# Optimization experiments

Measured on AMD Instinct MI355X. Metric: run time of the kernel, lower is better.

## Reference

```python
import jax, jax.numpy as jnp
import numpy as np

D = 1024
H = 16
HD = D // H  # 64


def setup_inputs() -> dict:
    key = jax.random.key(0)
    ks = jax.random.split(key, 10)
    s = 0.02
    return {
        "x": jax.random.normal(ks[0], (2, 2048, D), dtype=jnp.float32),
        "rel_bias": jax.random.normal(ks[1], (H, 2048, 2048), dtype=jnp.float32),
        "Wq": jax.random.normal(ks[2], (D, D), dtype=jnp.float32) * s,
        "bq": jnp.zeros((D,), dtype=jnp.float32),
        "Wk": jax.random.normal(ks[3], (D, D), dtype=jnp.float32) * s,
        "bk": jnp.zeros((D,), dtype=jnp.float32),
        "Wv": jax.random.normal(ks[4], (D, D), dtype=jnp.float32) * s,
        "bv": jnp.zeros((D,), dtype=jnp.float32),
        "Wo": jax.random.normal(ks[5], (D, D), dtype=jnp.float32) * s,
        "bo": jnp.zeros((D,), dtype=jnp.float32),
    }


def reference(x, rel_bias, Wq, bq, Wk, bk, Wv, bv, Wo, bo):
    B, L, _ = x.shape
    # QKV projections -> [B, H, L, HD]
    def proj(W, b):
        return (x @ W.T + b).reshape(B, L, H, HD).transpose(0, 2, 1, 3)
    q = proj(Wq, bq)
    k = proj(Wk, bk)
    v = proj(Wv, bv)
    scale = 1.0 / jnp.sqrt(jnp.float32(HD))
    scores = jnp.einsum("bhqd,bhkd->bhqk", q, k) * scale + rel_bias[None]
    attn = jax.nn.softmax(scores, axis=-1)  # dropout p=0 -> identity
    out = jnp.einsum("bhqk,bhkd->bhqd", attn, v)
    out = out.transpose(0, 2, 1, 3).reshape(B, L, H * HD)
    return out @ Wo.T + bo
```

## Files before the change

### kernel.cpp

```cpp
#include <hip/hip_runtime.h>


typedef __attribute__((ext_vector_type(8))) short bf16x8;
typedef __attribute__((ext_vector_type(4))) float f32x4;
typedef __attribute__((ext_vector_type(16))) float f32x16;
typedef __attribute__((ext_vector_type(8))) unsigned short u16x8;
using u16 = unsigned short;

#define MFMA16(a, b, c) __builtin_amdgcn_mfma_f32_16x16x32_bf16((a), (b), (c), 0, 0, 0)
#define MFMA32(a, b, c) __builtin_amdgcn_mfma_f32_32x32x16_bf16((a), (b), (c), 0, 0, 0)
#define LOG2E 1.44269504088896f
#define QSCALE (0.125f * 1.44269504088896f)

__device__ __forceinline__ u16 f2bf(float f) {
  union { float f; unsigned int u; } v; v.f = f;
  unsigned int r = v.u + 0x7FFFu + ((v.u >> 16) & 1u);
  return (u16)(r >> 16);
}

__device__ __forceinline__ unsigned cvt_pk_bf16(float lo, float hi) {
  unsigned r;
  asm volatile("v_cvt_pk_bf16_f32 %0, %1, %2" : "=v"(r) : "v"(lo), "v"(hi));
  return r;
}

__device__ __forceinline__ void pl32swap(unsigned& a, unsigned& b) {
#if __has_builtin(__builtin_amdgcn_permlane32_swap)
  typedef unsigned pl2 __attribute__((ext_vector_type(2)));
  pl2 r = __builtin_amdgcn_permlane32_swap(a, b, false, false);
  a = r[0];
  b = r[1];
#else
  asm volatile("v_permlane32_swap_b32 %0, %1" : "+v"(a), "+v"(b));
#endif
}

__device__ __forceinline__ void g2lds16(const void* gsrc, void* ldst) {
  __builtin_amdgcn_global_load_lds(
      (const __attribute__((address_space(1))) unsigned int*)gsrc,
      (__attribute__((address_space(3))) unsigned int*)ldst, 16, 0, 0);
}

__global__ __launch_bounds__(256) void cvt_all(
    const float* __restrict__ x, const float* __restrict__ wq,
    const float* __restrict__ wk, const float* __restrict__ wv,
    const float* __restrict__ wo, u16* __restrict__ xb,
    u16* __restrict__ w1b, u16* __restrict__ wob) {
  int bid = blockIdx.x, tid = threadIdx.x;
  const float* src; u16* dst; int i;
  if (bid < 2048)      { src = x;  dst = xb;            i = bid * 256 + tid; }
  else if (bid < 2560) { src = wq; dst = w1b;           i = (bid - 2048) * 256 + tid; }
  else if (bid < 3072) { src = wk; dst = w1b + (1<<20); i = (bid - 2560) * 256 + tid; }
  else if (bid < 3584) { src = wv; dst = w1b + (2<<20); i = (bid - 3072) * 256 + tid; }
  else                 { src = wo; dst = wob;           i = (bid - 3584) * 256 + tid; }
  const float4* s = (const float4*)src;
  float4 a = s[2 * i], b = s[2 * i + 1];
  u16x8 o;
  o[0] = f2bf(a.x); o[1] = f2bf(a.y); o[2] = f2bf(a.z); o[3] = f2bf(a.w);
  o[4] = f2bf(b.x); o[5] = f2bf(b.y); o[6] = f2bf(b.z); o[7] = f2bf(b.w);
  ((u16x8*)dst)[i] = o;
}

template <int MODE>
__global__ __launch_bounds__(256, 2) void gemm_bt(
    const u16* __restrict__ A, const u16* __restrict__ B,
    u16* __restrict__ qp, u16* __restrict__ kp, u16* __restrict__ vp,
    const float* __restrict__ b0, const float* __restrict__ b1,
    const float* __restrict__ b2, float* __restrict__ outp,
    const float* __restrict__ bo) {
  __shared__ __align__(16) u16 lA[128 * 64];
  __shared__ __align__(16) u16 lB[128 * 64];
  const int tid = threadIdx.x;
  const int lane = tid & 63, wid = tid >> 6;
  const int g = lane >> 4, cc = lane & 15;
  const int wr = wid >> 1, wc = wid & 1;
  const int m0 = blockIdx.y * 128, n0 = blockIdx.x * 128;
  f32x4 acc[4][4] = {};
  for (int kt = 0; kt < 16; ++kt) {
    const int kof = kt * 64;
#pragma unroll
    for (int i = 0; i < 4; ++i) {
      int cid = i * 256 + tid;
      int row = cid >> 3;
      int col = (cid & 7) * 8;
      g2lds16(A + (size_t)(m0 + row) * 1024 + kof + col, &lA[(i * 256 + wid * 64) * 8]);
      g2lds16(B + (size_t)(n0 + row) * 1024 + kof + col, &lB[(i * 256 + wid * 64) * 8]);
    }
    __syncthreads();
#pragma unroll
    for (int kc = 0; kc < 2; ++kc) {
      bf16x8 af[4], bfr[4];
#pragma unroll
      for (int mf = 0; mf < 4; ++mf)
        af[mf] = *(const bf16x8*)&lA[(wr * 64 + mf * 16 + cc) * 64 + kc * 32 + g * 8];
#pragma unroll
      for (int nf = 0; nf < 4; ++nf)
        bfr[nf] = *(const bf16x8*)&lB[(wc * 64 + nf * 16 + cc) * 64 + kc * 32 + g * 8];
#pragma unroll
      for (int mf = 0; mf < 4; ++mf)
#pragma unroll
        for (int nf = 0; nf < 4; ++nf)
          acc[mf][nf] = MFMA16(af[mf], bfr[nf], acc[mf][nf]);
    }
    __syncthreads();
  }
#pragma unroll
  for (int mf = 0; mf < 4; ++mf) {
#pragma unroll
    for (int nf = 0; nf < 4; ++nf) {
      int n = n0 + wc * 64 + nf * 16 + cc;
      if (MODE == 0) {
        int which = n >> 10;
        int nn = n & 1023;
        const float* bp = which == 0 ? b0 : (which == 1 ? b1 : b2);
        float bias = bp[nn];
        int h = nn >> 6, hd = nn & 63;
        int mb = m0 + wr * 64 + mf * 16 + g * 4;
        int bb = mb >> 11, ll0 = mb & 2047;
        if (which == 2) {
          ushort4 pk4;
          pk4.x = f2bf(acc[mf][nf][0] + bias);
          pk4.y = f2bf(acc[mf][nf][1] + bias);
          pk4.z = f2bf(acc[mf][nf][2] + bias);
          pk4.w = f2bf(acc[mf][nf][3] + bias);
          *(ushort4*)&vp[(((size_t)(bb * 16 + h)) * 64 + hd) * 2048 + ll0] = pk4;
        } else {
          u16* dp = which == 0 ? qp : kp;
#pragma unroll
          for (int r = 0; r < 4; ++r) {
            float val = acc[mf][nf][r] + bias;
            if (which == 0) val *= QSCALE;
            dp[(((size_t)(bb * 16 + h)) * 2048 + ll0 + r) * 64 + hd] = f2bf(val);
          }
        }
      } else {
        float bias = bo[n];
#pragma unroll
        for (int r = 0; r < 4; ++r) {
          int m = m0 + wr * 64 + mf * 16 + g * 4 + r;
          outp[(size_t)m * 1024 + n] = acc[mf][nf][r] + bias;
        }
      }
    }
  }
}

__global__ __launch_bounds__(256, 2) void attn_kernel(
    const u16* __restrict__ qm, const u16* __restrict__ km,
    const u16* __restrict__ vtm, const float* __restrict__ bias,
    u16* __restrict__ aout) {
  __shared__ __align__(16) u16 lK[2][4096];
  __shared__ __align__(16) u16 lV[2][4096];
  const int tid = threadIdx.x;
  const int lane = tid & 63, wid = tid >> 6;
  const int lq = lane & 31, hi = lane >> 5;
  const int lin = blockIdx.x;
  const int xcd = lin & 7, j = lin >> 3;
  const int h = xcd * 2 + (j >> 5);
  const int rem = j & 31;
  const int b = rem >> 4, qb = rem & 15;
  const int q0w = qb * 128 + wid * 32;
  const size_t bh = (size_t)b * 16 + h;
  const u16* kg = km + bh * 2048 * 64;
  const u16* vg = vtm + bh * 64 * 2048;
  const u16* qbase = qm + (bh * 2048 + q0w) * 64;
  const float* brow = bias + ((size_t)h * 2048 + q0w + lq) * 2048 + 4 * hi;

  bf16x8 qf[4];
#pragma unroll
  for (int i = 0; i < 4; ++i)
    qf[i] = *(const bf16x8*)&qbase[(size_t)lq * 64 + i * 16 + 8 * hi];

  f32x16 o[2];
#pragma unroll
  for (int r = 0; r < 16; ++r) { o[0][r] = 0.f; o[1][r] = 0.f; }
  float lsum = 0.f;

#define STAGE_TILE(gbase, rs, ldst)                                            \
  _Pragma("unroll") for (int rep = 0; rep < 2; ++rep) {                        \
    int i = rep * 256 + tid;                                                   \
    int row = i >> 3, pcol = i & 7;                                            \
    int lcol = pcol ^ (row & 7);                                               \
    g2lds16((gbase) + (size_t)row * (rs) + lcol * 8, (ldst) + i * 8);          \
  }

#define SUBTILE(s_, BC, PP)                                                    \
  {                                                                            \
    f32x16 acc;                                                                \
    _Pragma("unroll") for (int r = 0; r < 16; ++r) acc[r] = -32.0f;            \
    _Pragma("unroll") for (int i = 0; i < 4; ++i) {                            \
      int row = (s_) * 32 + lq;                                                \
      bf16x8 kf = *(const bf16x8*)&lK[PP][row * 64 + (((2 * i + hi) ^ (row & 7))) * 8]; \
      acc = MFMA32(kf, qf[i], acc);                                            \
    }                                                                          \
    _Pragma("unroll") for (int r = 0; r < 16; ++r)                             \
      acc[r] = fmaf(BC[(s_) * 4 + (r >> 2)][r & 3], LOG2E, acc[r]);            \
    float p[16];                                                               \
    _Pragma("unroll") for (int r = 0; r < 16; ++r) {                           \
      p[r] = __builtin_amdgcn_exp2f(acc[r]);                                   \
      lsum += p[r];                                                            \
    }                                                                          \
    unsigned c0 = cvt_pk_bf16(p[0], p[1]),   c1 = cvt_pk_bf16(p[2], p[3]);     \
    unsigned c2 = cvt_pk_bf16(p[4], p[5]),   c3 = cvt_pk_bf16(p[6], p[7]);     \
    unsigned c4 = cvt_pk_bf16(p[8], p[9]),   c5 = cvt_pk_bf16(p[10], p[11]);   \
    unsigned c6 = cvt_pk_bf16(p[12], p[13]), c7 = cvt_pk_bf16(p[14], p[15]);   \
    pl32swap(c0, c2); pl32swap(c1, c3);                   \
    pl32swap(c4, c6); pl32swap(c5, c7);                  \
    union { unsigned u[4]; bf16x8 v; } a0, a1;                                 \
    a0.u[0] = c0; a0.u[1] = c1; a0.u[2] = c2; a0.u[3] = c3;                    \
    a1.u[0] = c4; a1.u[1] = c5; a1.u[2] = c6; a1.u[3] = c7;                    \
    _Pragma("unroll") for (int dblk = 0; dblk < 2; ++dblk) {                   \
      int rowv = dblk * 32 + lq;                                               \
      bf16x8 v0 = *(const bf16x8*)&lV[PP][rowv * 64 + (((4 * (s_) + hi) ^ (rowv & 7))) * 8];     \
      bf16x8 v1 = *(const bf16x8*)&lV[PP][rowv * 64 + (((4 * (s_) + 2 + hi) ^ (rowv & 7))) * 8]; \
      o[dblk] = MFMA32(a0.v, v0, o[dblk]);                                     \
      o[dblk] = MFMA32(a1.v, v1, o[dblk]);                                     \
    }                                                                          \
  }

  float4 bA[8], bB[8];
  STAGE_TILE(kg, 64, (u16*)lK[0])
  STAGE_TILE(vg, 2048, (u16*)lV[0])
  __builtin_amdgcn_sched_barrier(0);
#pragma unroll
  for (int gi = 0; gi < 8; ++gi) {
    bA[gi] = *(const float4*)(brow + (gi >> 2) * 32 + (gi & 3) * 8);
    bB[gi] = *(const float4*)(brow + 64 + (gi >> 2) * 32 + (gi & 3) * 8);
  }
  __builtin_amdgcn_sched_barrier(0);
  asm volatile("s_waitcnt vmcnt(8)" ::: "memory");
  __builtin_amdgcn_sched_barrier(0);
  __builtin_amdgcn_s_barrier();
  __builtin_amdgcn_sched_barrier(0);

#define ATTN_STEP(kt_, BC, DOSTAGE, DOBIAS)                                    \
  {                                                                            \
    const int k0 = (kt_) * 64;                                                 \
    const int PP = (kt_) & 1;                                                  \
    if (DOSTAGE) {                                                             \
      STAGE_TILE(kg + (size_t)(k0 + 64) * 64, 64, (u16*)lK[PP ^ 1])            \
      STAGE_TILE(vg + (k0 + 64), 2048, (u16*)lV[PP ^ 1])                       \
    }                                                                          \
    __builtin_amdgcn_sched_barrier(0);                                         \
    SUBTILE(0, BC, PP)                                                         \
    SUBTILE(1, BC, PP)                                                         \
                          \
    if (DOBIAS) {                                                              \
      _Pragma("unroll") for (int gi = 0; gi < 8; ++gi)                         \
          BC[gi] = *(const float4*)(brow + k0 + 128 + (gi >> 2) * 32 + (gi & 3) * 8); \
    }                                                                          \
    __builtin_amdgcn_sched_barrier(0);                                         \
    if (DOSTAGE && DOBIAS) { asm volatile("s_waitcnt vmcnt(8)" ::: "memory"); }\
    else                   { asm volatile("s_waitcnt vmcnt(0)" ::: "memory"); }\
    __builtin_amdgcn_sched_barrier(0);                                         \
    if (DOSTAGE) { __builtin_amdgcn_s_barrier(); }                             \
    __builtin_amdgcn_sched_barrier(0);                                         \
  }

#pragma unroll 1
  for (int kt = 0; kt < 30; kt += 2) {
    ATTN_STEP(kt, bA, 1, 1)
    ATTN_STEP(kt + 1, bB, 1, 1)
  }
  ATTN_STEP(30, bA, 1, 0)
  ATTN_STEP(31, bB, 0, 0)
#undef ATTN_STEP
#undef SUBTILE
#undef STAGE_TILE

  lsum += __shfl_xor(lsum, 32, 64);
  float linv = 1.0f / lsum;
#pragma unroll
  for (int r = 0; r < 16; ++r) {
    int qr = (r & 3) + 8 * (r >> 2) + 4 * hi;
    float lr = __shfl(linv, qr, 64);
    size_t base = ((size_t)b * 2048 + q0w + qr) * 1024 + h * 64 + lq;
    aout[base] = f2bf(o[0][r] * lr);
    aout[base + 32] = f2bf(o[1][r] * lr);
  }
}

extern "C" void kernel_launch(void* const* d_in, const int* in_sizes, int n_in,
                              void* d_out, int out_size, void* d_ws, size_t ws_size,
                              hipStream_t stream) {
  const float* x  = (const float*)d_in[0];
  const float* rb = (const float*)d_in[1];
  const float* Wq = (const float*)d_in[2];
  const float* bq = (const float*)d_in[3];
  const float* Wk = (const float*)d_in[4];
  const float* bk = (const float*)d_in[5];
  const float* Wv = (const float*)d_in[6];
  const float* bv = (const float*)d_in[7];
  const float* Wo = (const float*)d_in[8];
  const float* bo = (const float*)d_in[9];
  float* out = (float*)d_out;
  char* ws = (char*)d_ws;

  u16* xb   = (u16*)(ws);
  u16* W1b  = (u16*)(ws + (8 << 20));
  u16* Wob  = (u16*)(ws + (14 << 20));
  u16* qb   = (u16*)(ws + (16 << 20));
  u16* kb2  = (u16*)(ws + (24 << 20));
  u16* vtb  = (u16*)(ws + (32 << 20));
  u16* aout = xb;

  cvt_all<<<4096, 256, 0, stream>>>(x, Wq, Wk, Wv, Wo, xb, W1b, Wob);
  gemm_bt<0><<<dim3(24, 32), 256, 0, stream>>>(xb, W1b, qb, kb2, vtb, bq, bk, bv,
                                               nullptr, nullptr);
  attn_kernel<<<512, 256, 0, stream>>>(qb, kb2, vtb, rb, aout);
  gemm_bt<1><<<dim3(8, 32), 256, 0, stream>>>(aout, Wob, nullptr, nullptr, nullptr,
                                              nullptr, nullptr, nullptr, out, bo);
}
```

Before: 175.2 us.

## Share relative-bias tiles across both batches via LDS in attention kernel

Each attention block now covers one head and query block for both batch entries, using 8 waves (two groups of four). The rel_bias tile for the current key step is staged once into LDS with swizzled async global-to-LDS copies, and both batch groups read it from there. Before, each batch read it separately from global memory into registers. This halves global traffic for the largest input. In exchange, each block needs 128KB of LDS, which limits occupancy to one block per CU, and the pipeline now waits for all loads to finish every step instead of keeping bias loads in flight.

```diff
diff --git a/kernel.cpp b/kernel.cpp
--- a/kernel.cpp
+++ b/kernel.cpp
@@ -145,26 +145,27 @@
   }
 }
 
-__global__ __launch_bounds__(256, 2) void attn_kernel(
+__global__ __launch_bounds__(512, 2) void attn_kernel(
     const u16* __restrict__ qm, const u16* __restrict__ km,
     const u16* __restrict__ vtm, const float* __restrict__ bias,
     u16* __restrict__ aout) {
-  __shared__ __align__(16) u16 lK[2][4096];
-  __shared__ __align__(16) u16 lV[2][4096];
+  __shared__ __align__(16) unsigned char smem[131072];
   const int tid = threadIdx.x;
   const int lane = tid & 63, wid = tid >> 6;
   const int lq = lane & 31, hi = lane >> 5;
+  const int s = wid & 3, b = wid >> 2;
   const int lin = blockIdx.x;
   const int xcd = lin & 7, j = lin >> 3;
-  const int h = xcd * 2 + (j >> 5);
-  const int rem = j & 31;
-  const int b = rem >> 4, qb = rem & 15;
-  const int q0w = qb * 128 + wid * 32;
+  const int h = xcd * 2 + (j >> 4);
+  const int qb = j & 15;
+  const int q0 = qb * 128;
+  const u16* kg0 = km + ((size_t)0 * 16 + h) * 2048 * 64;
+  const u16* kg1 = km + ((size_t)1 * 16 + h) * 2048 * 64;
+  const u16* vg0 = vtm + ((size_t)0 * 16 + h) * 64 * 2048;
+  const u16* vg1 = vtm + ((size_t)1 * 16 + h) * 64 * 2048;
+  const float* bg = bias + (size_t)h * 2048 * 2048;
   const size_t bh = (size_t)b * 16 + h;
-  const u16* kg = km + bh * 2048 * 64;
-  const u16* vg = vtm + bh * 64 * 2048;
-  const u16* qbase = qm + (bh * 2048 + q0w) * 64;
-  const float* brow = bias + ((size_t)h * 2048 + q0w + lq) * 2048 + 4 * hi;
+  const u16* qbase = qm + (bh * 2048 + q0 + s * 32) * 64;
 
   bf16x8 qf[4];
 #pragma unroll
@@ -176,97 +177,95 @@
   for (int r = 0; r < 16; ++r) { o[0][r] = 0.f; o[1][r] = 0.f; }
   float lsum = 0.f;
 
-#define STAGE_TILE(gbase, rs, ldst)                                            \
-  _Pragma("unroll") for (int rep = 0; rep < 2; ++rep) {                        \
-    int i = rep * 256 + tid;                                                   \
-    int row = i >> 3, pcol = i & 7;                                            \
-    int lcol = pcol ^ (row & 7);                                               \
-    g2lds16((gbase) + (size_t)row * (rs) + lcol * 8, (ldst) + i * 8);          \
-  }
-
-#define SUBTILE(s_, BC, PP)                                                    \
+#define STAGE_HP(P, k0n)                                                       \
   {                                                                            \
+    unsigned char* bdst = smem + (P) * 32768;                                  \
+    unsigned char* kdst = smem + 65536 + (P) * 16384;                          \
+    unsigned char* vdst = smem + 98304 + (P) * 16384;                          \
+    _Pragma("unroll") for (int i = 0; i < 4; ++i) {                            \
+      int slot = i * 512 + tid;                                                \
+      int row = slot >> 4, ch = slot & 15;                                     \
+      g2lds16(bg + (size_t)(q0 + row) * 2048 + (k0n) + ((ch ^ (row & 15)) << 2), \
+              bdst + slot * 16);                                               \
+    }                                                                          \
+    {                                                                          \
+      int kr = tid >> 3, ch = tid & 7;                                         \
+      int co = ((ch ^ (kr & 7)) << 3);                                         \
+      g2lds16(kg0 + (size_t)((k0n) + kr) * 64 + co, kdst + tid * 16);          \
+      g2lds16(kg1 + (size_t)((k0n) + kr) * 64 + co, kdst + 8192 + tid * 16);   \
+    }                                                                          \
+    {                                                                          \
+      int d = tid >> 3, ch = tid & 7;                                          \
+      int co = ((ch ^ (d & 7)) << 3);                                          \
+      g2lds16(vg0 + (size_t)d * 2048 + (k0n) + co, vdst + tid * 16);           \
+      g2lds16(vg1 + (size_t)d * 2048 + (k0n) + co, vdst + 8192 + tid * 16);    \
+    }                                                                          \
+  }
+
+#define SUBTILE(s_, PP)                                                        \
+  {                                                                            \
+    const u16* lKp = (const u16*)(smem + 65536 + (PP) * 16384 + b * 8192);     \
+    const u16* lVp = (const u16*)(smem + 98304 + (PP) * 16384 + b * 8192);     \
+    const float4* lB = (const float4*)(smem + (PP) * 32768);                   \
     f32x16 acc;                                                                \
     _Pragma("unroll") for (int r = 0; r < 16; ++r) acc[r] = -32.0f;            \
+    const int krow = (s_) * 32 + lq;                                           \
     _Pragma("unroll") for (int i = 0; i < 4; ++i) {                            \
-      int row = (s_) * 32 + lq;                                                \
-      bf16x8 kf = *(const bf16x8*)&lK[PP][row * 64 + (((2 * i + hi) ^ (row & 7))) * 8]; \
+      bf16x8 kf = *(const bf16x8*)&lKp[krow * 64 + (((2 * i + hi) ^ (krow & 7))) * 8]; \
       acc = MFMA32(kf, qf[i], acc);                                            \
     }                                                                          \
-    _Pragma("unroll") for (int r = 0; r < 16; ++r)                             \
-      acc[r] = fmaf(BC[(s_) * 4 + (r >> 2)][r & 3], LOG2E, acc[r]);            \
-    float p[16];                                                               \
+    const int brow = s * 32 + lq;                                              \
+    _Pragma("unroll") for (int g = 0; g < 4; ++g) {                            \
+      float4 b4 = lB[brow * 16 + (((s_) * 8 + 2 * g + hi) ^ (brow & 15))];     \
+      acc[g * 4 + 0] = fmaf(b4.x, LOG2E, acc[g * 4 + 0]);                      \
+      acc[g * 4 + 1] = fmaf(b4.y, LOG2E, acc[g * 4 + 1]);                      \
+      acc[g * 4 + 2] = fmaf(b4.z, LOG2E, acc[g * 4 + 2]);                      \
+      acc[g * 4 + 3] = fmaf(b4.w, LOG2E, acc[g * 4 + 3]);                      \
+    }                                                                          \
     _Pragma("unroll") for (int r = 0; r < 16; ++r) {                           \
-      p[r] = __builtin_amdgcn_exp2f(acc[r]);                                   \
-      lsum += p[r];                                                            \
-    }                                                                          \
-    unsigned c0 = cvt_pk_bf16(p[0], p[1]),   c1 = cvt_pk_bf16(p[2], p[3]);     \
-    unsigned c2 = cvt_pk_bf16(p[4], p[5]),   c3 = cvt_pk_bf16(p[6], p[7]);     \
-    unsigned c4 = cvt_pk_bf16(p[8], p[9]),   c5 = cvt_pk_bf16(p[10], p[11]);   \
-    unsigned c6 = cvt_pk_bf16(p[12], p[13]), c7 = cvt_pk_bf16(p[14], p[15]);   \
-    pl32swap(c0, c2); pl32swap(c1, c3);                   \
-    pl32swap(c4, c6); pl32swap(c5, c7);                  \
+      acc[r] = __builtin_amdgcn_exp2f(acc[r]);                                 \
+      lsum += acc[r];                                                          \
+    }                                                                          \
+    unsigned c0 = cvt_pk_bf16(acc[0], acc[1]),   c1 = cvt_pk_bf16(acc[2], acc[3]);   \
+    unsigned c2 = cvt_pk_bf16(acc[4], acc[5]),   c3 = cvt_pk_bf16(acc[6], acc[7]);   \
+    unsigned c4 = cvt_pk_bf16(acc[8], acc[9]),   c5 = cvt_pk_bf16(acc[10], acc[11]); \
+    unsigned c6 = cvt_pk_bf16(acc[12], acc[13]), c7 = cvt_pk_bf16(acc[14], acc[15]); \
+    pl32swap(c0, c2); pl32swap(c1, c3);                                        \
+    pl32swap(c4, c6); pl32swap(c5, c7);                                        \
     union { unsigned u[4]; bf16x8 v; } a0, a1;                                 \
     a0.u[0] = c0; a0.u[1] = c1; a0.u[2] = c2; a0.u[3] = c3;                    \
     a1.u[0] = c4; a1.u[1] = c5; a1.u[2] = c6; a1.u[3] = c7;                    \
     _Pragma("unroll") for (int dblk = 0; dblk < 2; ++dblk) {                   \
       int rowv = dblk * 32 + lq;                                               \
-      bf16x8 v0 = *(const bf16x8*)&lV[PP][rowv * 64 + (((4 * (s_) + hi) ^ (rowv & 7))) * 8];     \
-      bf16x8 v1 = *(const bf16x8*)&lV[PP][rowv * 64 + (((4 * (s_) + 2 + hi) ^ (rowv & 7))) * 8]; \
+      bf16x8 v0 = *(const bf16x8*)&lVp[rowv * 64 + (((4 * (s_) + hi) ^ (rowv & 7))) * 8];     \
+      bf16x8 v1 = *(const bf16x8*)&lVp[rowv * 64 + (((4 * (s_) + 2 + hi) ^ (rowv & 7))) * 8]; \
       o[dblk] = MFMA32(a0.v, v0, o[dblk]);                                     \
       o[dblk] = MFMA32(a1.v, v1, o[dblk]);                                     \
     }                                                                          \
   }
 
-  float4 bA[8], bB[8];
-  STAGE_TILE(kg, 64, (u16*)lK[0])
-  STAGE_TILE(vg, 2048, (u16*)lV[0])
+  STAGE_HP(0, 0)
   __builtin_amdgcn_sched_barrier(0);
-#pragma unroll
-  for (int gi = 0; gi < 8; ++gi) {
-    bA[gi] = *(const float4*)(brow + (gi >> 2) * 32 + (gi & 3) * 8);
-    bB[gi] = *(const float4*)(brow + 64 + (gi >> 2) * 32 + (gi & 3) * 8);
-  }
-  __builtin_amdgcn_sched_barrier(0);
-  asm volatile("s_waitcnt vmcnt(8)" ::: "memory");
+  asm volatile("s_waitcnt vmcnt(0)" ::: "memory");
   __builtin_amdgcn_sched_barrier(0);
   __builtin_amdgcn_s_barrier();
   __builtin_amdgcn_sched_barrier(0);
 
-#define ATTN_STEP(kt_, BC, DOSTAGE, DOBIAS)                                    \
-  {                                                                            \
-    const int k0 = (kt_) * 64;                                                 \
-    const int PP = (kt_) & 1;                                                  \
-    if (DOSTAGE) {                                                             \
-      STAGE_TILE(kg + (size_t)(k0 + 64) * 64, 64, (u16*)lK[PP ^ 1])            \
-      STAGE_TILE(vg + (k0 + 64), 2048, (u16*)lV[PP ^ 1])                       \
-    }                                                                          \
-    __builtin_amdgcn_sched_barrier(0);                                         \
-    SUBTILE(0, BC, PP)                                                         \
-    SUBTILE(1, BC, PP)                                                         \
-                          \
-    if (DOBIAS) {                                                              \
-      _Pragma("unroll") for (int gi = 0; gi < 8; ++gi)                         \
-          BC[gi] = *(const float4*)(brow + k0 + 128 + (gi >> 2) * 32 + (gi & 3) * 8); \
-    }                                                                          \
-    __builtin_amdgcn_sched_barrier(0);                                         \
-    if (DOSTAGE && DOBIAS) { asm volatile("s_waitcnt vmcnt(8)" ::: "memory"); }\
-    else                   { asm volatile("s_waitcnt vmcnt(0)" ::: "memory"); }\
-    __builtin_amdgcn_sched_barrier(0);                                         \
-    if (DOSTAGE) { __builtin_amdgcn_s_barrier(); }                             \
-    __builtin_amdgcn_sched_barrier(0);                                         \
-  }
-
 #pragma unroll 1
-  for (int kt = 0; kt < 30; kt += 2) {
-    ATTN_STEP(kt, bA, 1, 1)
-    ATTN_STEP(kt + 1, bB, 1, 1)
-  }
-  ATTN_STEP(30, bA, 1, 0)
-  ATTN_STEP(31, bB, 0, 0)
-#undef ATTN_STEP
+  for (int kt = 0; kt < 32; ++kt) {
+    const int P = kt & 1;
+    if (kt < 31) { STAGE_HP(P ^ 1, (kt + 1) * 64) }
+    __builtin_amdgcn_sched_barrier(0);
+    SUBTILE(0, P)
+    SUBTILE(1, P)
+    __builtin_amdgcn_sched_barrier(0);
+    asm volatile("s_waitcnt vmcnt(0)" ::: "memory");
+    __builtin_amdgcn_sched_barrier(0);
+    __builtin_amdgcn_s_barrier();
+    __builtin_amdgcn_sched_barrier(0);
+  }
 #undef SUBTILE
-#undef STAGE_TILE
+#undef STAGE_HP
 
   lsum += __shfl_xor(lsum, 32, 64);
   float linv = 1.0f / lsum;
@@ -274,7 +273,7 @@
   for (int r = 0; r < 16; ++r) {
     int qr = (r & 3) + 8 * (r >> 2) + 4 * hi;
     float lr = __shfl(linv, qr, 64);
-    size_t base = ((size_t)b * 2048 + q0w + qr) * 1024 + h * 64 + lq;
+    size_t base = ((size_t)b * 2048 + q0 + s * 32 + qr) * 1024 + h * 64 + lq;
     aout[base] = f2bf(o[0][r] * lr);
     aout[base + 32] = f2bf(o[1][r] * lr);
   }
@@ -307,7 +306,7 @@
   cvt_all<<<4096, 256, 0, stream>>>(x, Wq, Wk, Wv, Wo, xb, W1b, Wob);
   gemm_bt<0><<<dim3(24, 32), 256, 0, stream>>>(xb, W1b, qb, kb2, vtb, bq, bk, bv,
                                                nullptr, nullptr);
-  attn_kernel<<<512, 256, 0, stream>>>(qb, kb2, vtb, rb, aout);
+  attn_kernel<<<256, 512, 0, stream>>>(qb, kb2, vtb, rb, aout);
   gemm_bt<1><<<dim3(8, 32), 256, 0, stream>>>(aout, Wob, nullptr, nullptr, nullptr,
                                               nullptr, nullptr, nullptr, out, bo);
 }
```

Measured after the change: 163.1 us. 6.9% less time.
